# Performance work log

Hardware: AMD Instinct MI355X
Metric: run time of the kernel (lower is better)

## Reference

```python
import jax, jax.numpy as jnp
import numpy as np

B = 32768
T = 1024  # num_time_bins


def setup_inputs() -> dict:
    key = jax.random.key(0)
    k1, k2, k3, k4 = jax.random.split(key, 4)
    hazard_values = jax.random.uniform(k1, (B, T), dtype=jnp.float32)
    labels_Y = jax.random.uniform(k2, (B,), dtype=jnp.float32) * T
    # nn.Linear(T, T): weight [T, T] (out, in), bias [T]
    lim = 1.0 / np.sqrt(T)
    W = jax.random.uniform(k3, (T, T), minval=-lim, maxval=lim, dtype=jnp.float32)
    b = jax.random.uniform(k4, (T,), minval=-lim, maxval=lim, dtype=jnp.float32)
    return {"hazard_values": hazard_values, "labels_Y": labels_Y, "W": W, "b": b}


def reference(hazard_values, labels_Y, W, b):
    # linear + sigmoid + argmax -> per-row truncation position
    logits = hazard_values @ W.T + b                       # [B, T]
    trunc_pos = jnp.argmax(jax.nn.sigmoid(logits), axis=1, keepdims=True)  # [B, 1] int
    # survival curve
    S = jnp.cumprod(1.0 - hazard_values, axis=1)           # [B, T]
    # vectorized truncation decay: for t >= p, multiply by exp(-(t - p))
    t = jnp.arange(T)[None, :]                             # [1, T]
    decay = jnp.where(t >= trunc_pos,
                      jnp.exp(-(t - trunc_pos).astype(S.dtype)),
                      jnp.ones((), S.dtype))
    S = S * decay
    # MSE between argmax position and labels (original prints; we skip prints)
    p = trunc_pos[:, 0].astype(jnp.float32)
    truncation_loss = jnp.mean((p - labels_Y) ** 2)
    return trunc_pos, S, truncation_loss
```

## Files before the change

kernel.cpp:

```cpp
#include <hip/hip_runtime.h>

#define B_ROWS 32768
#define T_BINS 1024

typedef __attribute__((ext_vector_type(8))) _Float16 half8;
typedef __attribute__((ext_vector_type(4))) float floatx4;

__device__ __forceinline__ unsigned long long pack_max(float v, int col) {
    unsigned x = __float_as_uint(v);
    x = (x & 0x80000000u) ? ~x : (x | 0x80000000u);
    return ((unsigned long long)x << 32) | (unsigned)(~col);
}

__device__ __forceinline__ void async16h(const _Float16* g, _Float16* l) {
    __builtin_amdgcn_global_load_lds(
        (const __attribute__((address_space(1))) unsigned int*)g,
        (__attribute__((address_space(3))) unsigned int*)l,
        16, 0, 0);
}

__global__ __launch_bounds__(256) void tof16_kernel(
    const float* __restrict__ src, _Float16* __restrict__ dst, int n4)
{
    int idx = blockIdx.x * 256 + threadIdx.x;
    if (idx >= n4) return;
    float4 x = ((const float4*)src)[idx];
    union { _Float16 h[4]; ushort4 u; } cv;
    cv.h[0] = (_Float16)x.x;
    cv.h[1] = (_Float16)x.y;
    cv.h[2] = (_Float16)x.z;
    cv.h[3] = (_Float16)x.w;
    ((ushort4*)dst)[idx] = cv.u;
}

__global__ __launch_bounds__(512, 4) void mega_kernel(
    const float* __restrict__ A, const _Float16* __restrict__ Wh,
    const float* __restrict__ bias, const float* __restrict__ labels,
    float* __restrict__ out_trunc, float* __restrict__ out_S,
    float* __restrict__ loss_acc)
{
    __shared__ _Float16 sA[2][64 * 64];
    __shared__ _Float16 sW[2][256 * 64];

    const int tid  = threadIdx.x;
    const int lane = tid & 63;
    const int w    = tid >> 6;
    const int by   = blockIdx.x;

    const int arow = tid >> 3;
    const int c8   = tid & 7;
    const int x8a  = (arow ^ (arow >> 3)) & 7;
    const int asc  = c8 ^ x8a;
    const float* Abase = A + (size_t)(by * 64 + arow) * T_BINS + asc * 8;
    const int sAw  = arow * 64 + c8 * 8;

    const int l3  = lane >> 3;
    const int wsl = lane & 7;
    const int w4  = (w & 1) * 4;

    const int l15 = lane & 15;
    const int hi  = lane >> 4;
    const int xc  = (l15 & 7) ^ (l15 >> 3);

    float run_best[4][4];
    int   run_col[4][4];
#pragma unroll
    for (int i = 0; i < 4; ++i)
#pragma unroll
        for (int r = 0; r < 4; ++r) { run_best[i][r] = -3.4e38f; run_col[i][r] = 0; }

    {
        float4 f0 = *(const float4*)(Abase + 0);
        float4 f1 = *(const float4*)(Abase + 4);
        half8 hv;
        hv[0] = (_Float16)f0.x; hv[1] = (_Float16)f0.y; hv[2] = (_Float16)f0.z; hv[3] = (_Float16)f0.w;
        hv[4] = (_Float16)f1.x; hv[5] = (_Float16)f1.y; hv[6] = (_Float16)f1.z; hv[7] = (_Float16)f1.w;
        *(half8*)&sA[0][sAw] = hv;
    }
#pragma unroll
    for (int r = 0; r < 4; ++r)
        async16h(Wh + (size_t)(w * 32 + r * 8 + l3) * T_BINS + ((wsl ^ l3 ^ w4 ^ r) * 8),
                 &sW[0][(w * 32 + r * 8) * 64]);
    float4 pa0 = *(const float4*)(Abase + 64);
    float4 pa1 = *(const float4*)(Abase + 68);
    __syncthreads();

    int n = 0;
    for (int bx = 0; bx < 4; ++bx) {
        const int colbase = bx * 256 + w * 32 + l15;
        float bj[2];
        bj[0] = bias[colbase];
        bj[1] = bias[colbase + 16];

        floatx4 acc[4][2];
#pragma unroll
        for (int i = 0; i < 4; ++i)
#pragma unroll
            for (int j = 0; j < 2; ++j) acc[i][j] = (floatx4){0.f, 0.f, 0.f, 0.f};

        for (int t = 0; t < 16; ++t, ++n) {
            const int cur = n & 1;
            const int nxt = cur ^ 1;

            if (n < 63) {
                const int m   = n + 1;
                const int bxn = m >> 4;
                const int k0n = (m & 15) * 64;

#pragma unroll
                for (int r = 0; r < 4; ++r)
                    async16h(Wh + (size_t)(bxn * 256 + w * 32 + r * 8 + l3) * T_BINS
                                + k0n + ((wsl ^ l3 ^ w4 ^ r) * 8),
                             &sW[nxt][(w * 32 + r * 8) * 64]);

                const int kq = ((n + 2) & 15) * 64;
                float4 qa0 = *(const float4*)(Abase + kq + 0);
                float4 qa1 = *(const float4*)(Abase + kq + 4);

                {
                    half8 hv;
                    hv[0] = (_Float16)pa0.x; hv[1] = (_Float16)pa0.y;
                    hv[2] = (_Float16)pa0.z; hv[3] = (_Float16)pa0.w;
                    hv[4] = (_Float16)pa1.x; hv[5] = (_Float16)pa1.y;
                    hv[6] = (_Float16)pa1.z; hv[7] = (_Float16)pa1.w;
                    *(half8*)&sA[nxt][sAw] = hv;
                }
                pa0 = qa0; pa1 = qa1;
            }

#pragma unroll
            for (int g = 0; g < 2; ++g) {
                half8 ah[4], whf[2];
#pragma unroll
                for (int i = 0; i < 4; ++i)
                    ah[i] = *(const half8*)&sA[cur][(i * 16 + l15) * 64
                                                    + (((g * 4 + hi) ^ xc ^ (i * 2)) * 8)];
#pragma unroll
                for (int j = 0; j < 2; ++j)
                    whf[j] = *(const half8*)&sW[cur][(w * 32 + j * 16 + l15) * 64
                                                     + (((g * 4 + hi) ^ xc ^ (j * 2) ^ w4) * 8)];
#pragma unroll
                for (int i = 0; i < 4; ++i)
#pragma unroll
                    for (int j = 0; j < 2; ++j)
                        acc[i][j] = __builtin_amdgcn_mfma_f32_16x16x32_f16(ah[i], whf[j], acc[i][j], 0, 0, 0);
            }

            __syncthreads();
        }

#pragma unroll
        for (int i = 0; i < 4; ++i)
#pragma unroll
            for (int r = 0; r < 4; ++r)
#pragma unroll
                for (int j = 0; j < 2; ++j) {
                    float v = acc[i][j][r] + bj[j];
                    if (v > run_best[i][r]) { run_best[i][r] = v; run_col[i][r] = colbase + j * 16; }
                }
    }

    unsigned long long (*cand)[64] = reinterpret_cast<unsigned long long (*)[64]>(&sA[0][0]);
    float* trunc_s = reinterpret_cast<float*>(&sA[0][0]) + 1024;

#pragma unroll
    for (int i = 0; i < 4; ++i)
#pragma unroll
        for (int r = 0; r < 4; ++r) {
            float best = run_best[i][r];
            int   bc   = run_col[i][r];
#pragma unroll
            for (int off = 8; off >= 1; off >>= 1) {
                float ov = __shfl_xor(best, off, 64);
                int   oc = __shfl_xor(bc, off, 64);
                if (ov > best || (ov == best && oc < bc)) { best = ov; bc = oc; }
            }
            if (l15 == 0)
                cand[w][i * 16 + hi * 4 + r] = pack_max(best, bc);
        }
    __syncthreads();

    if (tid < 64) {
        unsigned long long m01 = cand[0][tid] > cand[1][tid] ? cand[0][tid] : cand[1][tid];
        unsigned long long m23 = cand[2][tid] > cand[3][tid] ? cand[2][tid] : cand[3][tid];
        unsigned long long m45 = cand[4][tid] > cand[5][tid] ? cand[4][tid] : cand[5][tid];
        unsigned long long m67 = cand[6][tid] > cand[7][tid] ? cand[6][tid] : cand[7][tid];
        unsigned long long ma  = m01 > m23 ? m01 : m23;
        unsigned long long mb  = m45 > m67 ? m45 : m67;
        unsigned long long mm  = ma > mb ? ma : mb;
        unsigned col = ~(unsigned)mm;
        float p = (float)col;
        int rowG = by * 64 + tid;
        out_trunc[rowG] = p;
        trunc_s[tid] = p;
        float d = p - labels[rowG];
        float term = d * d * (1.0f / (float)B_ROWS);
#pragma unroll
        for (int off = 32; off >= 1; off >>= 1)
            term += __shfl_down(term, off, 64);
        if (tid == 0) atomicAdd(loss_acc, term);
    }
    __syncthreads();

    for (int rr = 0; rr < 8; ++rr) {
        int row  = w * 8 + rr;
        int rowG = by * 64 + row;
        const float* Hrow = A + (size_t)rowG * T_BINS + lane * 16;
        float4 h0 = *(const float4*)(Hrow + 0);
        float4 h1 = *(const float4*)(Hrow + 4);
        float4 h2 = *(const float4*)(Hrow + 8);
        float4 h3 = *(const float4*)(Hrow + 12);
        float hv[16] = {h0.x, h0.y, h0.z, h0.w, h1.x, h1.y, h1.z, h1.w,
                        h2.x, h2.y, h2.z, h2.w, h3.x, h3.y, h3.z, h3.w};
        float vprod[16];
        float run = 1.f;
#pragma unroll
        for (int j = 0; j < 16; ++j) { run *= (1.f - hv[j]); vprod[j] = run; }
        float x = run;
#pragma unroll
        for (int off = 1; off < 64; off <<= 1) {
            float o = __shfl_up(x, off, 64);
            if (lane >= off) x *= o;
        }
        float pre = __shfl_up(x, 1, 64);
        if (lane == 0) pre = 1.f;

        int p  = (int)trunc_s[row];
        int t0 = lane * 16;
        float sv[16];
#pragma unroll
        for (int j = 0; j < 16; ++j) {
            float s = pre * vprod[j];
            int t = t0 + j;
            if (t >= p) s *= __expf((float)(p - t));
            sv[j] = s;
        }
        float* Srow = out_S + (size_t)rowG * T_BINS + lane * 16;
        *(float4*)(Srow + 0)  = (float4){sv[0],  sv[1],  sv[2],  sv[3]};
        *(float4*)(Srow + 4)  = (float4){sv[4],  sv[5],  sv[6],  sv[7]};
        *(float4*)(Srow + 8)  = (float4){sv[8],  sv[9],  sv[10], sv[11]};
        *(float4*)(Srow + 12) = (float4){sv[12], sv[13], sv[14], sv[15]};
    }
}

#define BMf 64
#define BKf 16
#define LDSS (BMf + 4)
__global__ __launch_bounds__(256) void gemm_argmax_fp32(
    const float* __restrict__ A, const float* __restrict__ W,
    const float* __restrict__ bias, unsigned long long* __restrict__ rec)
{
    __shared__ float As[BKf][LDSS];
    __shared__ float Ws[BKf][LDSS];
    const int tid = threadIdx.x;
    const int tx = tid & 15, ty = tid >> 4;
    const int bx = blockIdx.x, by = blockIdx.y;
    const int ar = tid >> 2, ak = (tid & 3) << 2;
    const float* Arow = A + (size_t)(by * BMf + ar) * T_BINS + ak;
    const float* Wrow = W + (size_t)(bx * BMf + ar) * T_BINS + ak;
    float acc[4][4];
#pragma unroll
    for (int i = 0; i < 4; ++i)
#pragma unroll
        for (int j = 0; j < 4; ++j) acc[i][j] = 0.f;
    for (int k0 = 0; k0 < T_BINS; k0 += BKf) {
        float4 av = *(const float4*)(Arow + k0);
        float4 wvv = *(const float4*)(Wrow + k0);
        As[ak + 0][ar] = av.x; As[ak + 1][ar] = av.y; As[ak + 2][ar] = av.z; As[ak + 3][ar] = av.w;
        Ws[ak + 0][ar] = wvv.x; Ws[ak + 1][ar] = wvv.y; Ws[ak + 2][ar] = wvv.z; Ws[ak + 3][ar] = wvv.w;
        __syncthreads();
#pragma unroll
        for (int k = 0; k < BKf; ++k) {
            float4 a4 = *(const float4*)&As[k][ty * 4];
            float4 w4 = *(const float4*)&Ws[k][tx * 4];
            float aa[4] = {a4.x, a4.y, a4.z, a4.w};
            float ww[4] = {w4.x, w4.y, w4.z, w4.w};
#pragma unroll
            for (int i = 0; i < 4; ++i)
#pragma unroll
                for (int j = 0; j < 4; ++j) acc[i][j] = fmaf(aa[i], ww[j], acc[i][j]);
        }
        __syncthreads();
    }
    const int colBase = bx * BMf + tx * 4;
    float bv[4];
#pragma unroll
    for (int j = 0; j < 4; ++j) bv[j] = bias[colBase + j];
#pragma unroll
    for (int i = 0; i < 4; ++i) {
        float best = acc[i][0] + bv[0];
        int bc = colBase;
#pragma unroll
        for (int j = 1; j < 4; ++j) {
            float v = acc[i][j] + bv[j];
            if (v > best) { best = v; bc = colBase + j; }
        }
#pragma unroll
        for (int off = 8; off >= 1; off >>= 1) {
            float ov = __shfl_xor(best, off, 64);
            int oc = __shfl_xor(bc, off, 64);
            if (ov > best || (ov == best && oc < bc)) { best = ov; bc = oc; }
        }
        if (tx == 0) atomicMax(&rec[by * BMf + ty * 4 + i], pack_max(best, bc));
    }
}

__global__ __launch_bounds__(256) void finalize_kernel(
    const unsigned long long* __restrict__ rec, const float* __restrict__ labels,
    float* __restrict__ out_trunc, float* __restrict__ loss_acc)
{
    int i = blockIdx.x * 256 + threadIdx.x;
    unsigned col = ~(unsigned)(rec[i] & 0xFFFFFFFFull);
    float p = (float)col;
    out_trunc[i] = p;
    float d = p - labels[i];
    float term = d * d * (1.0f / (float)B_ROWS);
#pragma unroll
    for (int off = 32; off >= 1; off >>= 1)
        term += __shfl_down(term, off, 64);
    __shared__ float partials[4];
    int lane = threadIdx.x & 63, wv = threadIdx.x >> 6;
    if (lane == 0) partials[wv] = term;
    __syncthreads();
    if (threadIdx.x == 0)
        atomicAdd(loss_acc, partials[0] + partials[1] + partials[2] + partials[3]);
}

__global__ __launch_bounds__(256) void scan_kernel_f32(
    const float* __restrict__ H, const float* __restrict__ trunc_f,
    float* __restrict__ Sout)
{
    const int row = blockIdx.x;
    const int tid = threadIdx.x;
    const int lane = tid & 63;
    const int wv = tid >> 6;
    const float4 h = *(const float4*)(H + (size_t)row * T_BINS + tid * 4);
    float l0 = 1.f - h.x;
    float l1 = l0 * (1.f - h.y);
    float l2 = l1 * (1.f - h.z);
    float l3 = l2 * (1.f - h.w);
    float x = l3;
#pragma unroll
    for (int off = 1; off < 64; off <<= 1) {
        float o = __shfl_up(x, off, 64);
        if (lane >= off) x *= o;
    }
    float ex = __shfl_up(x, 1, 64);
    if (lane == 0) ex = 1.f;
    __shared__ float wtot[4];
    if (lane == 63) wtot[wv] = x;
    __syncthreads();
    float wpre = 1.f;
#pragma unroll
    for (int w = 0; w < 3; ++w)
        if (w < wv) wpre *= wtot[w];
    float pre = wpre * ex;
    int p = (int)trunc_f[row];
    int t0 = tid * 4;
    float sv[4] = {pre * l0, pre * l1, pre * l2, pre * l3};
#pragma unroll
    for (int j = 0; j < 4; ++j) {
        int t = t0 + j;
        if (t >= p) sv[j] *= __expf((float)(p - t));
    }
    float4 s4 = {sv[0], sv[1], sv[2], sv[3]};
    *(float4*)(Sout + (size_t)row * T_BINS + tid * 4) = s4;
}

extern "C" void kernel_launch(void* const* d_in, const int* in_sizes, int n_in,
                              void* d_out, int out_size, void* d_ws, size_t ws_size,
                              hipStream_t stream)
{
    const float* hazard = (const float*)d_in[0];
    const float* labels = (const float*)d_in[1];
    const float* W      = (const float*)d_in[2];
    const float* bias   = (const float*)d_in[3];

    float* out       = (float*)d_out;
    float* out_trunc = out;
    float* out_S     = out + B_ROWS;
    float* out_loss  = out + B_ROWS + (size_t)B_ROWS * T_BINS;

    hipMemsetAsync(out_loss, 0, sizeof(float), stream);

    const size_t NW = (size_t)T_BINS * T_BINS;
    if (ws_size >= NW * sizeof(_Float16)) {
        _Float16* Wh = (_Float16*)d_ws;
        tof16_kernel<<<(int)(NW / 4 / 256), 256, 0, stream>>>(W, Wh, (int)(NW / 4));
        mega_kernel<<<B_ROWS / 64, 512, 0, stream>>>(
            hazard, Wh, bias, labels, out_trunc, out_S, out_loss);
    } else {
        unsigned long long* rec = (unsigned long long*)out_S;
        hipMemsetAsync(rec, 0, (size_t)B_ROWS * sizeof(unsigned long long), stream);
        dim3 ggrid(T_BINS / BMf, B_ROWS / BMf);
        gemm_argmax_fp32<<<ggrid, 256, 0, stream>>>(hazard, W, bias, rec);
        finalize_kernel<<<B_ROWS / 256, 256, 0, stream>>>(rec, labels, out_trunc, out_loss);
        scan_kernel_f32<<<B_ROWS, 256, 0, stream>>>(hazard, out_trunc, out_S);
    }
}
```

Measured before the change: 347.0 us.

## Load W fragments directly from global into registers, drop W LDS staging

Weight tiles are no longer staged through shared memory with async global-to-LDS loads. Each wave now loads its own W MFMA fragments straight from global memory into registers, prefetched one iteration ahead. Per-iteration __syncthreads is replaced by an LDS-only waitcnt plus a raw barrier, so outstanding global loads can stay in flight across the barrier. This cuts LDS footprint and LDS read traffic, but the W global loads are less coalesced (16-byte chunks per row) and the loop now issues one wasted prefetch on the last iteration.

```diff
diff --git a/kernel.cpp b/kernel.cpp
--- a/kernel.cpp
+++ b/kernel.cpp
@@ -10,13 +10,6 @@
     unsigned x = __float_as_uint(v);
     x = (x & 0x80000000u) ? ~x : (x | 0x80000000u);
     return ((unsigned long long)x << 32) | (unsigned)(~col);
-}
-
-__device__ __forceinline__ void async16h(const _Float16* g, _Float16* l) {
-    __builtin_amdgcn_global_load_lds(
-        (const __attribute__((address_space(1))) unsigned int*)g,
-        (__attribute__((address_space(3))) unsigned int*)l,
-        16, 0, 0);
 }
 
 __global__ __launch_bounds__(256) void tof16_kernel(
@@ -40,7 +33,8 @@
     float* __restrict__ loss_acc)
 {
     __shared__ _Float16 sA[2][64 * 64];
-    __shared__ _Float16 sW[2][256 * 64];
+    __shared__ unsigned long long cand[8][64];
+    __shared__ float trunc_s[64];
 
     const int tid  = threadIdx.x;
     const int lane = tid & 63;
@@ -54,13 +48,12 @@
     const float* Abase = A + (size_t)(by * 64 + arow) * T_BINS + asc * 8;
     const int sAw  = arow * 64 + c8 * 8;
 
-    const int l3  = lane >> 3;
-    const int wsl = lane & 7;
-    const int w4  = (w & 1) * 4;
-
     const int l15 = lane & 15;
     const int hi  = lane >> 4;
     const int xc  = (l15 & 7) ^ (l15 >> 3);
+
+    const _Float16* Wrow0 = Wh + (size_t)(w * 32 + l15) * T_BINS + hi * 8;
+    const _Float16* Wrow1 = Wh + (size_t)(w * 32 + 16 + l15) * T_BINS + hi * 8;
 
     float run_best[4][4];
     int   run_col[4][4];
@@ -77,13 +70,14 @@
         hv[4] = (_Float16)f1.x; hv[5] = (_Float16)f1.y; hv[6] = (_Float16)f1.z; hv[7] = (_Float16)f1.w;
         *(half8*)&sA[0][sAw] = hv;
     }
-#pragma unroll
-    for (int r = 0; r < 4; ++r)
-        async16h(Wh + (size_t)(w * 32 + r * 8 + l3) * T_BINS + ((wsl ^ l3 ^ w4 ^ r) * 8),
-                 &sW[0][(w * 32 + r * 8) * 64]);
+    half8 wf00 = *(const half8*)(Wrow0 + 0);
+    half8 wf01 = *(const half8*)(Wrow1 + 0);
+    half8 wf10 = *(const half8*)(Wrow0 + 32);
+    half8 wf11 = *(const half8*)(Wrow1 + 32);
     float4 pa0 = *(const float4*)(Abase + 64);
     float4 pa1 = *(const float4*)(Abase + 68);
-    __syncthreads();
+    asm volatile("s_waitcnt lgkmcnt(0)" ::: "memory");
+    __builtin_amdgcn_s_barrier();
 
     int n = 0;
     for (int bx = 0; bx < 4; ++bx) {
@@ -101,52 +95,50 @@
         for (int t = 0; t < 16; ++t, ++n) {
             const int cur = n & 1;
             const int nxt = cur ^ 1;
-
-            if (n < 63) {
-                const int m   = n + 1;
-                const int bxn = m >> 4;
-                const int k0n = (m & 15) * 64;
-
-#pragma unroll
-                for (int r = 0; r < 4; ++r)
-                    async16h(Wh + (size_t)(bxn * 256 + w * 32 + r * 8 + l3) * T_BINS
-                                + k0n + ((wsl ^ l3 ^ w4 ^ r) * 8),
-                             &sW[nxt][(w * 32 + r * 8) * 64]);
-
-                const int kq = ((n + 2) & 15) * 64;
-                float4 qa0 = *(const float4*)(Abase + kq + 0);
-                float4 qa1 = *(const float4*)(Abase + kq + 4);
-
-                {
-                    half8 hv;
-                    hv[0] = (_Float16)pa0.x; hv[1] = (_Float16)pa0.y;
-                    hv[2] = (_Float16)pa0.z; hv[3] = (_Float16)pa0.w;
-                    hv[4] = (_Float16)pa1.x; hv[5] = (_Float16)pa1.y;
-                    hv[6] = (_Float16)pa1.z; hv[7] = (_Float16)pa1.w;
-                    *(half8*)&sA[nxt][sAw] = hv;
-                }
-                pa0 = qa0; pa1 = qa1;
+            const int m   = (n + 1) & 63;
+            const int bxn = m >> 4;
+            const int k0n = (m & 15) * 64;
+
+            const size_t wkoff = (size_t)(bxn * 256) * T_BINS + k0n;
+            half8 wq00 = *(const half8*)(Wrow0 + wkoff + 0);
+            half8 wq01 = *(const half8*)(Wrow1 + wkoff + 0);
+            half8 wq10 = *(const half8*)(Wrow0 + wkoff + 32);
+            half8 wq11 = *(const half8*)(Wrow1 + wkoff + 32);
+
+            const int kq = ((n + 2) & 15) * 64;
+            float4 qa0 = *(const float4*)(Abase + kq + 0);
+            float4 qa1 = *(const float4*)(Abase + kq + 4);
+
+            {
+                half8 hv;
+                hv[0] = (_Float16)pa0.x; hv[1] = (_Float16)pa0.y;
+                hv[2] = (_Float16)pa0.z; hv[3] = (_Float16)pa0.w;
+                hv[4] = (_Float16)pa1.x; hv[5] = (_Float16)pa1.y;
+                hv[6] = (_Float16)pa1.z; hv[7] = (_Float16)pa1.w;
+                *(half8*)&sA[nxt][sAw] = hv;
             }
+            pa0 = qa0; pa1 = qa1;
 
 #pragma unroll
             for (int g = 0; g < 2; ++g) {
-                half8 ah[4], whf[2];
+                half8 ah[4];
 #pragma unroll
                 for (int i = 0; i < 4; ++i)
                     ah[i] = *(const half8*)&sA[cur][(i * 16 + l15) * 64
                                                     + (((g * 4 + hi) ^ xc ^ (i * 2)) * 8)];
-#pragma unroll
-                for (int j = 0; j < 2; ++j)
-                    whf[j] = *(const half8*)&sW[cur][(w * 32 + j * 16 + l15) * 64
-                                                     + (((g * 4 + hi) ^ xc ^ (j * 2) ^ w4) * 8)];
-#pragma unroll
-                for (int i = 0; i < 4; ++i)
-#pragma unroll
-                    for (int j = 0; j < 2; ++j)
-                        acc[i][j] = __builtin_amdgcn_mfma_f32_16x16x32_f16(ah[i], whf[j], acc[i][j], 0, 0, 0);
+                half8 w0 = g ? wf10 : wf00;
+                half8 w1 = g ? wf11 : wf01;
+#pragma unroll
+                for (int i = 0; i < 4; ++i) {
+                    acc[i][0] = __builtin_amdgcn_mfma_f32_16x16x32_f16(ah[i], w0, acc[i][0], 0, 0, 0);
+                    acc[i][1] = __builtin_amdgcn_mfma_f32_16x16x32_f16(ah[i], w1, acc[i][1], 0, 0, 0);
+                }
             }
 
-            __syncthreads();
+            wf00 = wq00; wf01 = wq01; wf10 = wq10; wf11 = wq11;
+
+            asm volatile("s_waitcnt lgkmcnt(0)" ::: "memory");
+            __builtin_amdgcn_s_barrier();
         }
 
 #pragma unroll
@@ -159,9 +151,6 @@
                     if (v > run_best[i][r]) { run_best[i][r] = v; run_col[i][r] = colbase + j * 16; }
                 }
     }
-
-    unsigned long long (*cand)[64] = reinterpret_cast<unsigned long long (*)[64]>(&sA[0][0]);
-    float* trunc_s = reinterpret_cast<float*>(&sA[0][0]) + 1024;
 
 #pragma unroll
     for (int i = 0; i < 4; ++i)
```

Measured after the change: 388.9 us. +12.1%, slower.
